# Optimization experiments

Hardware: AMD Instinct MI355X
Metric: run time of the kernel (lower is better)

Reference implementation:

```python
import jax, jax.numpy as jnp
import numpy as np

N = 4096        # nodes
E = 131072      # edges (avg degree 32)
IN = 512        # in_channels
HID = 512       # hidden_channels
HEADS = 4       # GAT heads
LAYERS = 3      # residual GCN layers
G = 16          # graphs in batch
OUT = 1         # out_channels
NEG_SLOPE = 0.2 # GAT LeakyReLU slope


def setup_inputs() -> dict:
    key = jax.random.key(0)
    ks = jax.random.split(key, 9)
    s = 0.02
    x = jax.random.normal(ks[0], (N, IN), dtype=jnp.float32)
    edge_index = jax.random.randint(ks[1], (2, E), 0, N)
    batch = jnp.sort(jax.random.randint(ks[2], (N,), 0, G))
    W_gat = jax.random.normal(ks[3], (HEADS, IN, HID), dtype=jnp.float32) * s
    a_src = jax.random.normal(ks[4], (HEADS, HID), dtype=jnp.float32) * s
    a_dst = jax.random.normal(ks[5], (HEADS, HID), dtype=jnp.float32) * s
    W_gcn = jax.random.normal(ks[6], (LAYERS, HID, HID), dtype=jnp.float32) * s
    fc_w = jax.random.normal(ks[7], (HID, OUT), dtype=jnp.float32) * s
    fc_b = jnp.zeros((OUT,), dtype=jnp.float32)
    return {"x": x, "edge_index": edge_index, "batch": batch,
            "W_gat": W_gat, "a_src": a_src, "a_dst": a_dst,
            "W_gcn": W_gcn, "fc_w": fc_w, "fc_b": fc_b}


def reference(x, edge_index, batch, W_gat, a_src, a_dst, W_gcn, fc_w, fc_b):
    src, dst = edge_index[0], edge_index[1]

    # ---- LatentRelationCapturerGAT: multi-head GAT, one output per head ----
    h = jnp.einsum('nc,hcd->nhd', x, W_gat)                    # [N,H,D]
    lg_src = jnp.einsum('nhd,hd->nh', h, a_src)                # [N,H]
    lg_dst = jnp.einsum('nhd,hd->nh', h, a_dst)                # [N,H]
    e = jax.nn.leaky_relu(lg_src[src] + lg_dst[dst], NEG_SLOPE)  # [E,H]
    # segment softmax over incoming edges of each destination node
    m = jax.ops.segment_max(e, dst, num_segments=N)            # [N,H]
    w = jnp.exp(e - m[dst])                                    # [E,H]
    z = jax.ops.segment_sum(w, dst, num_segments=N)            # [N,H]
    alpha = w / (z[dst] + 1e-16)                               # [E,H]
    H0 = jax.ops.segment_sum(alpha[:, :, None] * h[src], dst, num_segments=N)  # [N,H,D]

    # ---- dense adjacency build + GCN normalization (shared across heads) ----
    A = jnp.zeros((N, N), dtype=x.dtype).at[src, dst].set(1.0)
    A = A + jnp.eye(N, dtype=x.dtype)                          # self-loops
    dinv = jax.lax.rsqrt(jnp.sum(A, axis=1))                   # deg >= 1
    A_hat = dinv[:, None] * A * dinv[None, :]                  # D^-1/2 (A+I) D^-1/2

    # ---- DeepResidualGCN: H <- relu(A_hat @ H @ W_l) + H (heads batched) ----
    H = H0
    for l in range(W_gcn.shape[0]):
        P = jnp.einsum('nm,mhd->nhd', A_hat, H)                # propagate
        H = jax.nn.relu(jnp.einsum('nhd,de->nhe', P, W_gcn[l])) + H

    # ---- per-head global mean pool, then mean over heads ----
    ones = jnp.ones((N,), dtype=x.dtype)
    cnt = jnp.maximum(jax.ops.segment_sum(ones, batch, num_segments=G), 1.0)  # [G]
    pooled = jax.ops.segment_sum(H, batch, num_segments=G) / cnt[:, None, None]  # [G,H,D]
    feats = pooled.mean(axis=1)                                # [G,D]

    return feats @ fc_w + fc_b                                 # [G,OUT]
```

## Files before the change

kernel.cpp:

```cpp
#include <hip/hip_runtime.h>
#include <cstdint>
#include <cstddef>

#define Nn    4096
#define Ee    131072
#define INC   512
#define HIDC  512
#define HEADS 4
#define NLAY  3
#define GG    16
#define FW    2048

typedef __attribute__((ext_vector_type(8))) short bfrag;
typedef __attribute__((ext_vector_type(4))) float ffrag;

__device__ __forceinline__ ushort f2bf(float v){
  uint u = __builtin_bit_cast(uint, v);
  u += 0x7fffu + ((u>>16)&1u);
  return (ushort)(u>>16);
}
__device__ __forceinline__ float bf2f(ushort s){
  uint u = ((uint)s)<<16; return __builtin_bit_cast(float, u);
}
__device__ __forceinline__ void fma8(float* acc, uint4 g, float w){
  uint u[4] = {g.x, g.y, g.z, g.w};
  #pragma unroll
  for (int q=0;q<4;q++){
    float lo = __builtin_bit_cast(float, u[q]<<16);
    float hi = __builtin_bit_cast(float, u[q] & 0xffff0000u);
    acc[2*q]   += w*lo;
    acc[2*q+1] += w*hi;
  }
}
__device__ __forceinline__ uint4 pack8(const float* a){
  uint4 o;
  o.x = (uint)f2bf(a[0]) | ((uint)f2bf(a[1])<<16);
  o.y = (uint)f2bf(a[2]) | ((uint)f2bf(a[3])<<16);
  o.z = (uint)f2bf(a[4]) | ((uint)f2bf(a[5])<<16);
  o.w = (uint)f2bf(a[6]) | ((uint)f2bf(a[7])<<16);
  return o;
}

__global__ __launch_bounds__(256) void tobf(const float* __restrict__ X, ushort* __restrict__ Xb){
  int i = blockIdx.x*256 + threadIdx.x;
  Xb[i] = f2bf(X[i]);
}

__global__ __launch_bounds__(256) void tbf(const float* __restrict__ W, ushort* __restrict__ T){
  __shared__ float tile[32][33];
  int b = blockIdx.z;
  int r0 = blockIdx.y*32, c0 = blockIdx.x*32;
  int t = threadIdx.x;
  int i = t>>3, j0 = (t&7)*4;
  const float* Wb = W + (size_t)b*512*512;
  float4 v = *(const float4*)(Wb + (size_t)(r0+i)*512 + c0 + j0);
  tile[i][j0]=v.x; tile[i][j0+1]=v.y; tile[i][j0+2]=v.z; tile[i][j0+3]=v.w;
  __syncthreads();
  ushort* o = T + (size_t)b*512*512 + (size_t)(c0+i)*512 + r0 + j0;
  #pragma unroll
  for (int q=0;q<4;q++) o[q] = f2bf(tile[j0+q][i]);
}

__global__ __launch_bounds__(256) void gemm_bf(
    const ushort* __restrict__ A, const ushort* __restrict__ B,
    const float* __restrict__ Res, float* __restrict__ Cf, ushort* __restrict__ Cb,
    int M, int N, int K, int relu_res)
{
  __shared__ __align__(16) ushort Ah[4096];
  __shared__ __align__(16) ushort Bh[4096];
  int t = threadIdx.x;
  int m0 = blockIdx.y*128, n0 = blockIdx.x*128;
  int srow = t>>1, c = t&1, scol = c*16;
  int wave = t>>6, lane = t&63;
  int wm = (wave&1)*64, wn = (wave>>1)*64;
  int lm = lane&15, quad = lane>>4;

  ffrag acc[4][4];
  #pragma unroll
  for (int i=0;i<4;i++){
    #pragma unroll
    for (int j=0;j<4;j++) acc[i][j] = (ffrag){0.f,0.f,0.f,0.f};
  }

  const ushort* pA = A + (size_t)(m0+srow)*K + scol;
  const ushort* pB = B + (size_t)(n0+srow)*K + scol;

  uint4 ra0 = *(const uint4*)(pA);  uint4 ra1 = *(const uint4*)(pA+8);
  uint4 rb0 = *(const uint4*)(pB);  uint4 rb1 = *(const uint4*)(pB+8);

  int w0 = ((2*c)*128 + srow)*8;
  int w1 = w0 + 1024;
  for (int k0 = 0; k0 < K; k0 += 32){
    __syncthreads();
    *(uint4*)&Ah[w0] = ra0; *(uint4*)&Ah[w1] = ra1;
    *(uint4*)&Bh[w0] = rb0; *(uint4*)&Bh[w1] = rb1;
    __syncthreads();
    if (k0+32 < K){
      ra0 = *(const uint4*)(pA+k0+32); ra1 = *(const uint4*)(pA+k0+40);
      rb0 = *(const uint4*)(pB+k0+32); rb1 = *(const uint4*)(pB+k0+40);
    }
    bfrag af[4];
    #pragma unroll
    for (int mt=0; mt<4; mt++)
      af[mt] = *(const bfrag*)&Ah[(quad*128 + wm + mt*16 + lm)*8];
    #pragma unroll
    for (int nt=0; nt<4; nt++){
      bfrag bf = *(const bfrag*)&Bh[(quad*128 + wn + nt*16 + lm)*8];
      #pragma unroll
      for (int mt=0; mt<4; mt++)
        acc[mt][nt] = __builtin_amdgcn_mfma_f32_16x16x32_bf16(af[mt], bf, acc[mt][nt], 0,0,0);
    }
  }

  #pragma unroll
  for (int mt=0; mt<4; mt++){
    #pragma unroll
    for (int nt=0; nt<4; nt++){
      #pragma unroll
      for (int r=0;r<4;r++){
        int grow = m0 + wm + mt*16 + quad*4 + r;
        int gcol = n0 + wn + nt*16 + lm;
        size_t off = (size_t)grow*N + gcol;
        float v = acc[mt][nt][r];
        if (relu_res) v = fmaxf(v,0.f) + Res[off];
        if (Cf) Cf[off] = v;
        if (Cb) Cb[off] = f2bf(v);
      }
    }
  }
}

__global__ __launch_bounds__(256) void compute_lg(const ushort* __restrict__ hbf,
    const float* __restrict__ a_src, const float* __restrict__ a_dst,
    float* __restrict__ lgs, float* __restrict__ lgd){
  int n = blockIdx.x; int t = threadIdx.x;
  int hd = t>>6, lane = t&63;
  uint4 g = *(const uint4*)(hbf + (size_t)n*FW + hd*HIDC + lane*8);
  float h[8] = {0,0,0,0,0,0,0,0};
  fma8(h, g, 1.0f);
  float4 as0 = *(const float4*)(a_src + hd*HIDC + lane*8);
  float4 as1 = *(const float4*)(a_src + hd*HIDC + lane*8 + 4);
  float4 ad0 = *(const float4*)(a_dst + hd*HIDC + lane*8);
  float4 ad1 = *(const float4*)(a_dst + hd*HIDC + lane*8 + 4);
  float s1 = h[0]*as0.x + h[1]*as0.y + h[2]*as0.z + h[3]*as0.w
           + h[4]*as1.x + h[5]*as1.y + h[6]*as1.z + h[7]*as1.w;
  float s2 = h[0]*ad0.x + h[1]*ad0.y + h[2]*ad0.z + h[3]*ad0.w
           + h[4]*ad1.x + h[5]*ad1.y + h[6]*ad1.z + h[7]*ad1.w;
  for (int off=32; off; off>>=1){ s1 += __shfl_down(s1,off); s2 += __shfl_down(s2,off); }
  if (lane==0){ lgs[n*HEADS+hd]=s1; lgd[n*HEADS+hd]=s2; }
}

__global__ __launch_bounds__(256) void edge_pass1(const int* __restrict__ src, const int* __restrict__ dst,
    int* __restrict__ indeg, unsigned int* __restrict__ bitmap,
    int* __restrict__ cnt_s, int* __restrict__ flag){
  int e = blockIdx.x*256+threadIdx.x; if (e>=Ee) return;
  int s = src[e], d = dst[e];
  atomicAdd(&indeg[d],1);
  unsigned int key = (unsigned int)s*Nn + (unsigned int)d;
  unsigned int bit = 1u<<(key&31);
  unsigned int old = atomicOr(&bitmap[key>>5], bit);
  int f = (old & bit) ? 0 : 1;
  flag[e] = f;
  if (f) atomicAdd(&cnt_s[s],1);
}

__global__ __launch_bounds__(1024) void exscan2(const int* __restrict__ cnt0, int* __restrict__ rp0,
    const int* __restrict__ cnt1, int* __restrict__ rp1){
  const int* cnt = blockIdx.x ? cnt1 : cnt0;
  int* rowptr    = blockIdx.x ? rp1  : rp0;
  __shared__ int sums[1024];
  int t = threadIdx.x;
  int v[4]; int s=0;
  #pragma unroll
  for (int i=0;i<4;i++){ int idx=t*4+i; v[i] = cnt[idx]; s+=v[i]; }
  sums[t]=s; __syncthreads();
  for (int off=1; off<1024; off<<=1){
    int other = (t>=off)? sums[t-off] : 0;
    __syncthreads();
    sums[t] += other;
    __syncthreads();
  }
  int run = (t>0)? sums[t-1] : 0;
  #pragma unroll
  for (int i=0;i<4;i++){ int idx=t*4+i; rowptr[idx]=run; run+=v[i]; }
  if (t==1023) rowptr[Nn]=sums[1023];
}

__global__ __launch_bounds__(256) void compute_dinv(const int* __restrict__ cnt, float* __restrict__ dinv){
  int n = blockIdx.x*256+threadIdx.x; if (n<Nn) dinv[n] = 1.0f/sqrtf((float)(1+cnt[n]));
}

__global__ __launch_bounds__(256) void edge_pass2(const int* __restrict__ src, const int* __restrict__ dst,
    const int* __restrict__ flag,
    const int* __restrict__ rp_d, int* __restrict__ fill_d, int* __restrict__ slist,
    const int* __restrict__ rp_s, int* __restrict__ fill_s, int2* __restrict__ cw,
    const float* __restrict__ dinv){
  int e = blockIdx.x*256+threadIdx.x; if (e>=Ee) return;
  int s = src[e], d = dst[e];
  int p = atomicAdd(&fill_d[d],1); slist[rp_d[d]+p] = s;
  if (flag[e]){
    int q = atomicAdd(&fill_s[s],1);
    cw[rp_s[s]+q] = make_int2(d, __float_as_int(dinv[d]));
  }
}

__global__ __launch_bounds__(256) void gat_aggregate(const ushort* __restrict__ hbf,
    const float* __restrict__ lgs, const float* __restrict__ lgd,
    const int* __restrict__ rowptr, const int* __restrict__ slist,
    float* __restrict__ Hfeat, ushort* __restrict__ Hbf){
  int t = threadIdx.x;
  int wv = __builtin_amdgcn_readfirstlane(t>>6);
  int lane = t&63;
  int b = blockIdx.x;
  int hd = __builtin_amdgcn_readfirstlane(b & 3);
  int n = ((b>>2)<<2) + wv;
  int beg = rowptr[n], deg = rowptr[n+1]-beg;
  float ldst = lgd[n*HEADS+hd];
  float m_ = -3.4e38f, z_ = 0.f;
  int   s0 = 0; float v0 = 0.f;
  for (int i=lane; i<deg; i+=64){
    int s = slist[beg+i];
    float v = lgs[s*HEADS+hd] + ldst;
    v = v>0.f ? v : 0.2f*v;
    if (i<64){ s0=s; v0=v; }
    float mn = fmaxf(m_, v);
    z_ = z_*__expf(m_-mn) + __expf(v-mn);
    m_ = mn;
  }
  for (int o=32;o;o>>=1){
    float mo = __shfl_down(m_,o), zo = __shfl_down(z_,o);
    float mn = fmaxf(m_, mo);
    z_ = z_*__expf(m_-mn) + zo*__expf(mo-mn);
    m_ = mn;
  }
  float mx = __shfl(m_,0);
  float zs = __shfl(z_,0);
  float inv = 1.f/(zs+1e-16f);
  float acc[8] = {0,0,0,0,0,0,0,0};
  const ushort* hb = hbf + hd*HIDC + lane*8;
  for (int base=0; base<deg; base+=64){
    float al; int s;
    if (base==0){
      s = s0;
      al = (lane<deg) ? __expf(v0-mx)*inv : 0.f;
    } else {
      int i = base+lane;
      al = 0.f; s = 0;
      if (i<deg){
        s = slist[beg+i];
        float v = lgs[s*HEADS+hd] + ldst; v = v>0.f ? v : 0.2f*v;
        al = __expf(v-mx)*inv;
      }
    }
    int cn = min(64, deg-base);
    int c = 0;
    for (; c+4<=cn; c+=4){
      float a0=__shfl(al,c),   a1=__shfl(al,c+1), a2=__shfl(al,c+2), a3=__shfl(al,c+3);
      int   s0_=__shfl(s,c),   s1_=__shfl(s,c+1), s2_=__shfl(s,c+2), s3_=__shfl(s,c+3);
      uint4 g0 = *(const uint4*)(hb + (size_t)s0_*FW);
      uint4 g1 = *(const uint4*)(hb + (size_t)s1_*FW);
      uint4 g2 = *(const uint4*)(hb + (size_t)s2_*FW);
      uint4 g3 = *(const uint4*)(hb + (size_t)s3_*FW);
      fma8(acc, g0, a0); fma8(acc, g1, a1); fma8(acc, g2, a2); fma8(acc, g3, a3);
    }
    for (; c<cn; c++){
      float a = __shfl(al,c);
      int ss  = __shfl(s,c);
      uint4 g = *(const uint4*)(hb + (size_t)ss*FW);
      fma8(acc, g, a);
    }
  }
  size_t off = (size_t)n*FW + hd*HIDC + lane*8;
  *(float4*)(Hfeat + off)     = make_float4(acc[0],acc[1],acc[2],acc[3]);
  *(float4*)(Hfeat + off + 4) = make_float4(acc[4],acc[5],acc[6],acc[7]);
  *(uint4*)(Hbf + off) = pack8(acc);
}

__global__ __launch_bounds__(256) void spmm_bf(const ushort* __restrict__ Hbf,
    ushort* __restrict__ Phi,
    const int* __restrict__ rowptr, const int2* __restrict__ cw, const float* __restrict__ dinv){
  int t = threadIdx.x;
  int wv = __builtin_amdgcn_readfirstlane(t>>6);
  int lane = t&63;
  int b = blockIdx.x;
  int ck = __builtin_amdgcn_readfirstlane(b & 3);
  int n = ((b>>2)<<2) + wv;
  int f = (ck<<9) + lane*8;
  float di = dinv[n];
  float acc[8] = {0,0,0,0,0,0,0,0};
  const ushort* hb = Hbf + f;
  uint4 self = *(const uint4*)(hb + (size_t)n*FW);
  fma8(acc, self, di*di);
  int beg = rowptr[n], end = rowptr[n+1];
  for (int base=beg; base<end; base+=64){
    int i = base + lane;
    int m = n; float w = 0.f;
    if (i < end){ int2 e = cw[i]; m = e.x; w = di*__int_as_float(e.y); }
    int cn = min(64, end-base);
    int c = 0;
    for (; c+4<=cn; c+=4){
      int   m0=__shfl(m,c),   m1=__shfl(m,c+1), m2=__shfl(m,c+2), m3=__shfl(m,c+3);
      float w0=__shfl(w,c),   w1=__shfl(w,c+1), w2=__shfl(w,c+2), w3=__shfl(w,c+3);
      uint4 g0 = *(const uint4*)(hb + (size_t)m0*FW);
      uint4 g1 = *(const uint4*)(hb + (size_t)m1*FW);
      uint4 g2 = *(const uint4*)(hb + (size_t)m2*FW);
      uint4 g3 = *(const uint4*)(hb + (size_t)m3*FW);
      fma8(acc, g0, w0); fma8(acc, g1, w1); fma8(acc, g2, w2); fma8(acc, g3, w3);
    }
    for (; c<cn; c++){
      int mm   = __shfl(m,c);
      float ww = __shfl(w,c);
      uint4 g = *(const uint4*)(hb + (size_t)mm*FW);
      fma8(acc, g, ww);
    }
  }
  *(uint4*)(Phi + (size_t)n*FW + f) = pack8(acc);
}

__global__ __launch_bounds__(256) void graph_offsets(const int* __restrict__ batch, int* __restrict__ goff){
  __shared__ int cnt[GG];
  int t = threadIdx.x;
  if (t<GG) cnt[t]=0;
  __syncthreads();
  for (int i=t;i<Nn;i+=256) atomicAdd(&cnt[batch[i]],1);
  __syncthreads();
  if (t==0){ int run=0; for (int g=0; g<GG; g++){ goff[g]=run; run+=cnt[g]; } goff[GG]=run; }
}
__global__ __launch_bounds__(256) void pool_accum(const float* __restrict__ H,
    const int* __restrict__ batch, float* __restrict__ psum){
  int d = blockIdx.y*256 + threadIdx.x;
  int n0 = blockIdx.x*32;
  int g = batch[n0];
  float s = 0.f;
  for (int k=0;k<32;k++){
    int n = n0+k;
    int gn = batch[n];
    if (gn != g){ atomicAdd(&psum[(size_t)g*FW+d], s); s=0.f; g=gn; }
    s += H[(size_t)n*FW + d];
  }
  atomicAdd(&psum[(size_t)g*FW+d], s);
}
__global__ __launch_bounds__(256) void final_out(const float* __restrict__ psum,
    const int* __restrict__ goff,
    const float* __restrict__ fc_w, const float* __restrict__ fc_b, float* __restrict__ out){
  int g = blockIdx.x; int t = threadIdx.x;
  float cinv = 0.25f / fmaxf((float)(goff[g+1]-goff[g]), 1.f);
  float p = 0.f;
  for (int d=t; d<HIDC; d+=256){
    float f = cinv*(psum[(size_t)g*FW+d] + psum[(size_t)g*FW+HIDC+d]
                  + psum[(size_t)g*FW+2*HIDC+d] + psum[(size_t)g*FW+3*HIDC+d]);
    p += f*fc_w[d];
  }
  __shared__ float red[4];
  for (int off=32; off; off>>=1) p += __shfl_down(p,off);
  if ((t&63)==0) red[t>>6]=p;
  __syncthreads();
  if (t==0) out[g] = red[0]+red[1]+red[2]+red[3] + fc_b[0];
}

extern "C" void kernel_launch(void* const* d_in, const int* in_sizes, int n_in,
                              void* d_out, int out_size, void* d_ws, size_t ws_size,
                              hipStream_t stream){
  const float* x      = (const float*)d_in[0];
  const int*   ei     = (const int*)d_in[1];
  const int*   batch  = (const int*)d_in[2];
  const float* W_gat  = (const float*)d_in[3];
  const float* a_src  = (const float*)d_in[4];
  const float* a_dst  = (const float*)d_in[5];
  const float* W_gcn  = (const float*)d_in[6];
  const float* fc_w   = (const float*)d_in[7];
  const float* fc_b   = (const float*)d_in[8];
  float* out = (float*)d_out;
  const int* src = ei;
  const int* dst = ei + Ee;

  char* w = (char*)d_ws;
  size_t off = 0;
  auto alloc = [&](size_t bytes)->char*{ char* p = w + off; off = (off + bytes + 255) & ~(size_t)255; return p; };
  float*  Hfeat  = (float*)alloc((size_t)Nn*FW*4);
  ushort* hbf    = (ushort*)alloc((size_t)Nn*FW*2);
  ushort* Hbf    = (ushort*)alloc((size_t)Nn*FW*2);
  ushort* Xbf    = (ushort*)alloc((size_t)Nn*INC*2);
  ushort* WgatT  = (ushort*)alloc((size_t)HEADS*INC*HIDC*2);
  ushort* WgcnT  = (ushort*)alloc((size_t)NLAY*HIDC*HIDC*2);
  float* lgs    = (float*)alloc((size_t)Nn*HEADS*4);
  float* lgd    = (float*)alloc((size_t)Nn*HEADS*4);
  int* indeg    = (int*)alloc(Nn*4);
  int* rowptr_d = (int*)alloc((Nn+1)*4);
  int* slist    = (int*)alloc(Ee*4);
  int* fill_d   = (int*)alloc(Nn*4);
  unsigned int* bitmap = (unsigned int*)alloc((size_t)Nn*Nn/8);
  int* cnt_s    = (int*)alloc(Nn*4);
  int* rowptr_s = (int*)alloc((Nn+1)*4);
  int2* cwlist  = (int2*)alloc((size_t)Ee*8);
  int* fill_s   = (int*)alloc(Nn*4);
  int* flag     = (int*)alloc(Ee*4);
  float* dinv   = (float*)alloc(Nn*4);
  float* psum   = (float*)alloc((size_t)GG*FW*4);
  int* goff     = (int*)alloc((GG+1)*4);
  ushort* Phi   = hbf;

  hipMemsetAsync(indeg, 0, Nn*4, stream);
  hipMemsetAsync(fill_d, 0, Nn*4, stream);
  hipMemsetAsync(cnt_s, 0, Nn*4, stream);
  hipMemsetAsync(fill_s, 0, Nn*4, stream);
  hipMemsetAsync(bitmap, 0, (size_t)Nn*Nn/8, stream);
  hipMemsetAsync(psum, 0, (size_t)GG*FW*4, stream);

  tobf<<<(Nn*INC)/256,256,0,stream>>>(x, Xbf);
  tbf<<<dim3(16,16,HEADS),256,0,stream>>>(W_gat, WgatT);
  tbf<<<dim3(16,16,NLAY),256,0,stream>>>(W_gcn, WgcnT);

  gemm_bf<<<dim3(FW/128, Nn/128),256,0,stream>>>(Xbf, WgatT,
      nullptr, nullptr, hbf, Nn, FW, INC, 0);
  compute_lg<<<Nn,256,0,stream>>>(hbf, a_src, a_dst, lgs, lgd);

  edge_pass1<<<Ee/256,256,0,stream>>>(src, dst, indeg, bitmap, cnt_s, flag);
  exscan2<<<2,1024,0,stream>>>(indeg, rowptr_d, cnt_s, rowptr_s);
  compute_dinv<<<Nn/256,256,0,stream>>>(cnt_s, dinv);
  edge_pass2<<<Ee/256,256,0,stream>>>(src, dst, flag, rowptr_d, fill_d, slist,
                                      rowptr_s, fill_s, cwlist, dinv);
  gat_aggregate<<<Nn,256,0,stream>>>(hbf, lgs, lgd, rowptr_d, slist, Hfeat, Hbf);

  for (int l=0;l<NLAY;l++){
    spmm_bf<<<Nn,256,0,stream>>>(Hbf, Phi, rowptr_s, cwlist, dinv);
    gemm_bf<<<dim3(HIDC/128, (Nn*HEADS)/128),256,0,stream>>>(Phi,
        WgcnT + (size_t)l*HIDC*HIDC,
        Hfeat, Hfeat, (l==NLAY-1)? nullptr : Hbf, Nn*HEADS, HIDC, HIDC, 1);
  }

  graph_offsets<<<1,256,0,stream>>>(batch, goff);
  pool_accum<<<dim3(Nn/32, FW/256),256,0,stream>>>(Hfeat, batch, psum);
  final_out<<<GG,256,0,stream>>>(psum, goff, fc_w, fc_b, out);
}
```

Before: 407.6 us.

## Use direct global-to-LDS loads in GEMM, deepen gather unroll, add nontemporal stores, merge memsets

The bf16 GEMM now stages A and B tiles with global_load_lds, writing straight into shared memory instead of going through registers. This drops the register-held prefetch of the next K tile, so global loads no longer overlap with the MFMA work. The GAT aggregation and SpMM gather loops gain an 8-wide unrolled stage so more row loads are in flight to hide gather latency. Output stores in the GEMM, aggregation and SpMM kernels become nontemporal. The six zeroing memsets are merged into one by placing those buffers next to each other in the workspace.

```diff
diff --git a/kernel.cpp b/kernel.cpp
--- a/kernel.cpp
+++ b/kernel.cpp
@@ -13,6 +13,8 @@
 
 typedef __attribute__((ext_vector_type(8))) short bfrag;
 typedef __attribute__((ext_vector_type(4))) float ffrag;
+typedef __attribute__((ext_vector_type(4))) uint uint4v;
+typedef __attribute__((ext_vector_type(4))) float float4v;
 
 __device__ __forceinline__ ushort f2bf(float v){
   uint u = __builtin_bit_cast(uint, v);
@@ -32,13 +34,25 @@
     acc[2*q+1] += w*hi;
   }
 }
-__device__ __forceinline__ uint4 pack8(const float* a){
-  uint4 o;
-  o.x = (uint)f2bf(a[0]) | ((uint)f2bf(a[1])<<16);
-  o.y = (uint)f2bf(a[2]) | ((uint)f2bf(a[3])<<16);
-  o.z = (uint)f2bf(a[4]) | ((uint)f2bf(a[5])<<16);
-  o.w = (uint)f2bf(a[6]) | ((uint)f2bf(a[7])<<16);
-  return o;
+__device__ __forceinline__ void nt_store_u4(void* p, uint a, uint b, uint c, uint d){
+  uint4v x = {a,b,c,d};
+  __builtin_nontemporal_store(x, (uint4v*)p);
+}
+__device__ __forceinline__ void nt_store_f4(void* p, float a, float b, float c, float d){
+  float4v x = {a,b,c,d};
+  __builtin_nontemporal_store(x, (float4v*)p);
+}
+__device__ __forceinline__ void nt_pack8(void* p, const float* a){
+  nt_store_u4(p,
+    (uint)f2bf(a[0]) | ((uint)f2bf(a[1])<<16),
+    (uint)f2bf(a[2]) | ((uint)f2bf(a[3])<<16),
+    (uint)f2bf(a[4]) | ((uint)f2bf(a[5])<<16),
+    (uint)f2bf(a[6]) | ((uint)f2bf(a[7])<<16));
+}
+__device__ __forceinline__ void gload_lds16(const ushort* g, ushort* l){
+  __builtin_amdgcn_global_load_lds(
+      (const __attribute__((address_space(1))) void*)g,
+      (__attribute__((address_space(3))) void*)l, 16, 0, 0);
 }
 
 __global__ __launch_bounds__(256) void tobf(const float* __restrict__ X, ushort* __restrict__ Xb){
@@ -70,7 +84,6 @@
   __shared__ __align__(16) ushort Bh[4096];
   int t = threadIdx.x;
   int m0 = blockIdx.y*128, n0 = blockIdx.x*128;
-  int srow = t>>1, c = t&1, scol = c*16;
   int wave = t>>6, lane = t&63;
   int wm = (wave&1)*64, wn = (wave>>1)*64;
   int lm = lane&15, quad = lane>>4;
@@ -82,23 +95,21 @@
     for (int j=0;j<4;j++) acc[i][j] = (ffrag){0.f,0.f,0.f,0.f};
   }
 
-  const ushort* pA = A + (size_t)(m0+srow)*K + scol;
-  const ushort* pB = B + (size_t)(n0+srow)*K + scol;
-
-  uint4 ra0 = *(const uint4*)(pA);  uint4 ra1 = *(const uint4*)(pA+8);
-  uint4 rb0 = *(const uint4*)(pB);  uint4 rb1 = *(const uint4*)(pB+8);
-
-  int w0 = ((2*c)*128 + srow)*8;
-  int w1 = w0 + 1024;
+  const ushort* gA0 = A + (size_t)(m0 + lane)*K      + wave*8;
+  const ushort* gA1 = A + (size_t)(m0 + 64 + lane)*K + wave*8;
+  const ushort* gB0 = B + (size_t)(n0 + lane)*K      + wave*8;
+  const ushort* gB1 = B + (size_t)(n0 + 64 + lane)*K + wave*8;
+  ushort* lA0 = &Ah[(wave*128     )*8];
+  ushort* lA1 = &Ah[(wave*128 + 64)*8];
+  ushort* lB0 = &Bh[(wave*128     )*8];
+  ushort* lB1 = &Bh[(wave*128 + 64)*8];
+
   for (int k0 = 0; k0 < K; k0 += 32){
+    gload_lds16(gA0 + k0, lA0);
+    gload_lds16(gA1 + k0, lA1);
+    gload_lds16(gB0 + k0, lB0);
+    gload_lds16(gB1 + k0, lB1);
     __syncthreads();
-    *(uint4*)&Ah[w0] = ra0; *(uint4*)&Ah[w1] = ra1;
-    *(uint4*)&Bh[w0] = rb0; *(uint4*)&Bh[w1] = rb1;
-    __syncthreads();
-    if (k0+32 < K){
-      ra0 = *(const uint4*)(pA+k0+32); ra1 = *(const uint4*)(pA+k0+40);
-      rb0 = *(const uint4*)(pB+k0+32); rb1 = *(const uint4*)(pB+k0+40);
-    }
     bfrag af[4];
     #pragma unroll
     for (int mt=0; mt<4; mt++)
@@ -110,6 +121,7 @@
       for (int mt=0; mt<4; mt++)
         acc[mt][nt] = __builtin_amdgcn_mfma_f32_16x16x32_bf16(af[mt], bf, acc[mt][nt], 0,0,0);
     }
+    __syncthreads();
   }
 
   #pragma unroll
@@ -123,8 +135,8 @@
         size_t off = (size_t)grow*N + gcol;
         float v = acc[mt][nt][r];
         if (relu_res) v = fmaxf(v,0.f) + Res[off];
-        if (Cf) Cf[off] = v;
-        if (Cb) Cb[off] = f2bf(v);
+        if (Cf) __builtin_nontemporal_store(v, &Cf[off]);
+        if (Cb) __builtin_nontemporal_store(f2bf(v), &Cb[off]);
       }
     }
   }
@@ -254,14 +266,27 @@
     }
     int cn = min(64, deg-base);
     int c = 0;
+    for (; c+8<=cn; c+=8){
+      uint4 g[8]; float a[8];
+      #pragma unroll
+      for (int q=0;q<8;q++){
+        a[q] = __shfl(al,c+q);
+        int ss = __shfl(s,c+q);
+        g[q] = *(const uint4*)(hb + (size_t)ss*FW);
+      }
+      #pragma unroll
+      for (int q=0;q<8;q++) fma8(acc, g[q], a[q]);
+    }
     for (; c+4<=cn; c+=4){
-      float a0=__shfl(al,c),   a1=__shfl(al,c+1), a2=__shfl(al,c+2), a3=__shfl(al,c+3);
-      int   s0_=__shfl(s,c),   s1_=__shfl(s,c+1), s2_=__shfl(s,c+2), s3_=__shfl(s,c+3);
-      uint4 g0 = *(const uint4*)(hb + (size_t)s0_*FW);
-      uint4 g1 = *(const uint4*)(hb + (size_t)s1_*FW);
-      uint4 g2 = *(const uint4*)(hb + (size_t)s2_*FW);
-      uint4 g3 = *(const uint4*)(hb + (size_t)s3_*FW);
-      fma8(acc, g0, a0); fma8(acc, g1, a1); fma8(acc, g2, a2); fma8(acc, g3, a3);
+      uint4 g[4]; float a[4];
+      #pragma unroll
+      for (int q=0;q<4;q++){
+        a[q] = __shfl(al,c+q);
+        int ss = __shfl(s,c+q);
+        g[q] = *(const uint4*)(hb + (size_t)ss*FW);
+      }
+      #pragma unroll
+      for (int q=0;q<4;q++) fma8(acc, g[q], a[q]);
     }
     for (; c<cn; c++){
       float a = __shfl(al,c);
@@ -271,9 +296,9 @@
     }
   }
   size_t off = (size_t)n*FW + hd*HIDC + lane*8;
-  *(float4*)(Hfeat + off)     = make_float4(acc[0],acc[1],acc[2],acc[3]);
-  *(float4*)(Hfeat + off + 4) = make_float4(acc[4],acc[5],acc[6],acc[7]);
-  *(uint4*)(Hbf + off) = pack8(acc);
+  nt_store_f4(Hfeat + off,     acc[0],acc[1],acc[2],acc[3]);
+  nt_store_f4(Hfeat + off + 4, acc[4],acc[5],acc[6],acc[7]);
+  nt_pack8(Hbf + off, acc);
 }
 
 __global__ __launch_bounds__(256) void spmm_bf(const ushort* __restrict__ Hbf,
@@ -298,14 +323,27 @@
     if (i < end){ int2 e = cw[i]; m = e.x; w = di*__int_as_float(e.y); }
     int cn = min(64, end-base);
     int c = 0;
+    for (; c+8<=cn; c+=8){
+      uint4 g[8]; float ww[8];
+      #pragma unroll
+      for (int q=0;q<8;q++){
+        ww[q] = __shfl(w,c+q);
+        int mm = __shfl(m,c+q);
+        g[q] = *(const uint4*)(hb + (size_t)mm*FW);
+      }
+      #pragma unroll
+      for (int q=0;q<8;q++) fma8(acc, g[q], ww[q]);
+    }
     for (; c+4<=cn; c+=4){
-      int   m0=__shfl(m,c),   m1=__shfl(m,c+1), m2=__shfl(m,c+2), m3=__shfl(m,c+3);
-      float w0=__shfl(w,c),   w1=__shfl(w,c+1), w2=__shfl(w,c+2), w3=__shfl(w,c+3);
-      uint4 g0 = *(const uint4*)(hb + (size_t)m0*FW);
-      uint4 g1 = *(const uint4*)(hb + (size_t)m1*FW);
-      uint4 g2 = *(const uint4*)(hb + (size_t)m2*FW);
-      uint4 g3 = *(const uint4*)(hb + (size_t)m3*FW);
-      fma8(acc, g0, w0); fma8(acc, g1, w1); fma8(acc, g2, w2); fma8(acc, g3, w3);
+      uint4 g[4]; float ww[4];
+      #pragma unroll
+      for (int q=0;q<4;q++){
+        ww[q] = __shfl(w,c+q);
+        int mm = __shfl(m,c+q);
+        g[q] = *(const uint4*)(hb + (size_t)mm*FW);
+      }
+      #pragma unroll
+      for (int q=0;q<4;q++) fma8(acc, g[q], ww[q]);
     }
     for (; c<cn; c++){
       int mm   = __shfl(m,c);
@@ -314,7 +352,10 @@
       fma8(acc, g, ww);
     }
   }
-  *(uint4*)(Phi + (size_t)n*FW + f) = pack8(acc);
+  float a[8]; 
+  #pragma unroll
+  for (int q=0;q<8;q++) a[q]=acc[q];
+  nt_pack8(Phi + (size_t)n*FW + f, a);
 }
 
 __global__ __launch_bounds__(256) void graph_offsets(const int* __restrict__ batch, int* __restrict__ goff){
@@ -386,26 +427,22 @@
   float* lgs    = (float*)alloc((size_t)Nn*HEADS*4);
   float* lgd    = (float*)alloc((size_t)Nn*HEADS*4);
   int* indeg    = (int*)alloc(Nn*4);
+  int* fill_d   = (int*)alloc(Nn*4);
+  int* cnt_s    = (int*)alloc(Nn*4);
+  int* fill_s   = (int*)alloc(Nn*4);
+  float* psum   = (float*)alloc((size_t)GG*FW*4);
+  unsigned int* bitmap = (unsigned int*)alloc((size_t)Nn*Nn/8);
+  size_t zero_bytes = (size_t)Nn*4*4 + (size_t)GG*FW*4 + (size_t)Nn*Nn/8;
   int* rowptr_d = (int*)alloc((Nn+1)*4);
   int* slist    = (int*)alloc(Ee*4);
-  int* fill_d   = (int*)alloc(Nn*4);
-  unsigned int* bitmap = (unsigned int*)alloc((size_t)Nn*Nn/8);
-  int* cnt_s    = (int*)alloc(Nn*4);
   int* rowptr_s = (int*)alloc((Nn+1)*4);
   int2* cwlist  = (int2*)alloc((size_t)Ee*8);
-  int* fill_s   = (int*)alloc(Nn*4);
   int* flag     = (int*)alloc(Ee*4);
   float* dinv   = (float*)alloc(Nn*4);
-  float* psum   = (float*)alloc((size_t)GG*FW*4);
   int* goff     = (int*)alloc((GG+1)*4);
   ushort* Phi   = hbf;
 
-  hipMemsetAsync(indeg, 0, Nn*4, stream);
-  hipMemsetAsync(fill_d, 0, Nn*4, stream);
-  hipMemsetAsync(cnt_s, 0, Nn*4, stream);
-  hipMemsetAsync(fill_s, 0, Nn*4, stream);
-  hipMemsetAsync(bitmap, 0, (size_t)Nn*Nn/8, stream);
-  hipMemsetAsync(psum, 0, (size_t)GG*FW*4, stream);
+  hipMemsetAsync(indeg, 0, zero_bytes, stream);
 
   tobf<<<(Nn*INC)/256,256,0,stream>>>(x, Xbf);
   tbf<<<dim3(16,16,HEADS),256,0,stream>>>(W_gat, WgatT);
```

After: 459.6 us. 12.7% more time.
